# Kernel tuning notes

Measured on AMD Instinct MI355X. Metric: run time of the kernel, lower is better.

Reference implementation:

```python
import jax, jax.numpy as jnp
import numpy as np

PATCH_NUMS = (1, 2, 3, 4, 5, 6, 8, 10, 13, 16)
B = 8
NUM_HEADS = 24
HEAD_DIM = 64
C = NUM_HEADS * HEAD_DIM  # 1536
ROPE_BASE = 10000.0


def _position_ids(batch):
    # Mirrors get_position_ids: 2D grid coords per scale, rescaled to the largest grid.
    largest = PATCH_NUMS[-1]
    coords = []
    for pn in PATCH_NUMS:
        g = np.stack(np.meshgrid(np.arange(pn), np.arange(pn), indexing='ij'), axis=-1)
        coords.append((g.astype(np.float64) / pn * largest).reshape(-1, 2))
    pos = np.concatenate(coords, axis=0).astype(np.float32)  # [L, 2]
    return jnp.asarray(np.broadcast_to(pos, (batch,) + pos.shape))


def setup_inputs() -> dict:
    key = jax.random.key(0)
    k0, k1, k2 = jax.random.split(key, 3)
    L = sum(p * p for p in PATCH_NUMS)  # 680
    s = 0.02
    return {
        'x': jax.random.normal(k0, (B, L, C), jnp.float32),
        'pos_ids': _position_ids(B),                                   # [B, L, 2] float coords
        'w_qkv': jax.random.normal(k1, (3 * C, C), jnp.float32) * s,   # fused QKV weight (no bias in Linear)
        'q_bias': jnp.zeros((C,), jnp.float32),                        # learnable q bias
        'v_bias': jnp.zeros((C,), jnp.float32),                        # learnable v bias (k bias is fixed zero)
        'w_o': jax.random.normal(k2, (C, C), jnp.float32) * s,
        'b_o': jnp.zeros((C,), jnp.float32),
    }


def _rope_2d_cos_sin(pos_ids):
    # LlamaRotaryEmbedding (2D): inv_freq over head_dim with step 4; each spatial axis
    # gets head_dim/2 rotary channels laid out as [fx, fx, fy, fy] (rotate-half pairing).
    inv_freq = 1.0 / (ROPE_BASE ** (jnp.arange(0, HEAD_DIM, 4, dtype=jnp.float32) / HEAD_DIM))  # [hd/4]
    f = pos_ids[..., None] * inv_freq                      # [B, L, 2, hd/4]
    f2 = jnp.concatenate([f, f], axis=-1)                  # [B, L, 2, hd/2]
    emb = f2.reshape(f2.shape[0], f2.shape[1], HEAD_DIM)   # [B, L, hd]
    return jnp.cos(emb), jnp.sin(emb)


def _rotate_half(t):
    h = t.shape[-1] // 2
    return jnp.concatenate([-t[..., h:], t[..., :h]], axis=-1)


def reference(x, pos_ids, w_qkv, q_bias, v_bias, w_o, b_o):
    Bb, L, Cc = x.shape
    bias = jnp.concatenate([q_bias, jnp.zeros_like(q_bias), v_bias])  # zero k bias
    qkv = (x @ w_qkv.T + bias).reshape(Bb, L, 3, NUM_HEADS, HEAD_DIM)
    q, k, v = qkv[:, :, 0], qkv[:, :, 1], qkv[:, :, 2]  # bshd

    cos, sin = _rope_2d_cos_sin(pos_ids)                # [B, L, hd]
    cos = cos[:, :, None, :]                            # broadcast over heads (unsqueeze_dim=2)
    sin = sin[:, :, None, :]
    q = q * cos + _rotate_half(q) * sin
    k = k * cos + _rotate_half(k) * sin

    scale = 1.0 / jnp.sqrt(jnp.asarray(HEAD_DIM, jnp.float32))
    scores = jnp.einsum('bshd,bthd->bhst', q, k) * scale  # [B, H, L, L]
    attn = jax.nn.softmax(scores, axis=-1)
    out = jnp.einsum('bhst,bthd->bshd', attn, v).reshape(Bb, L, Cc)
    return out @ w_o.T + b_o
```

## Files before the change

### kernel.cpp

```cpp
#include <hip/hip_runtime.h>
#include <cmath>

typedef _Float16 f16;
typedef _Float16 f16x2 __attribute__((ext_vector_type(2)));
typedef _Float16 f16x4 __attribute__((ext_vector_type(4)));
typedef _Float16 f16x8 __attribute__((ext_vector_type(8)));
typedef float f32x4 __attribute__((ext_vector_type(4)));

namespace {

constexpr int kB = 8;
constexpr int kL = 680;
constexpr int kH = 24;
constexpr int kD = 64;
constexpr int kC = 1536;
constexpr int kM = kB * kL;
constexpr int kN3 = 3 * kC;
constexpr int kNKT = 11;
constexpr int kNQT = 6;

#define ASYNC_CP16(gp, lp)                                          \
  __builtin_amdgcn_global_load_lds(                                 \
      (const __attribute__((address_space(1))) unsigned int*)(gp),  \
      (__attribute__((address_space(3))) unsigned int*)(lp), 16, 0, 0)

__device__ inline int xcd_swizzle(int bid, int nwg) {
  int q = nwg >> 3, r = nwg & 7;
  int x = bid & 7, idx = bid >> 3;
  return (x < r ? x * (q + 1) : r * (q + 1) + (x - r) * q) + idx;
}

__device__ inline void stripe_decode(int id, int gx, int gy, int& mt,
                                     int& nt) {
  const int SW = 4;
  int nst = (gx + SW - 1) / SW;
  int s = id / (gy * SW);
  if (s > nst - 1) s = nst - 1;
  int rem = id - s * gy * SW;
  int w = gx - s * SW;
  if (w > SW) w = SW;
  mt = rem / w;
  nt = s * SW + rem % w;
}

__global__ void fused_cvt_bias(const float* __restrict__ x,
                               const float* __restrict__ wqkv,
                               const float* __restrict__ wo,
                               const float* __restrict__ qb,
                               const float* __restrict__ vb,
                               f16* __restrict__ x16,
                               f16* __restrict__ wqkv16,
                               f16* __restrict__ wo16,
                               float* __restrict__ bias) {
  const int c0 = kM * kC / 4, c1 = kN3 * kC / 4, c2 = kC * kC / 4,
            c3 = kN3 / 4;
  int i = blockIdx.x * blockDim.x + threadIdx.x;
  const float* src = nullptr;
  f16* dst = nullptr;
  if (i < c0) {
    src = x; dst = x16;
  } else if ((i -= c0) < c1) {
    src = wqkv; dst = wqkv16;
  } else if ((i -= c1) < c2) {
    src = wo; dst = wo16;
  } else if ((i -= c2) < c3) {
    int base = i * 4;
    float vv[4];
#pragma unroll
    for (int k2 = 0; k2 < 4; ++k2) {
      int idx = base + k2;
      float b = 0.0f;
      if (idx < kC) b = qb[idx];
      else if (idx >= 2 * kC) b = vb[idx - 2 * kC];
      vv[k2] = b;
    }
    *reinterpret_cast<float4*>(&bias[base]) =
        make_float4(vv[0], vv[1], vv[2], vv[3]);
    return;
  } else {
    return;
  }
  float4 v = *reinterpret_cast<const float4*>(&src[i * 4]);
  f16x4 o;
  o[0] = (f16)v.x; o[1] = (f16)v.y; o[2] = (f16)v.z; o[3] = (f16)v.w;
  *reinterpret_cast<f16x4*>(&dst[i * 4]) = o;
}

__global__ void reduce_add(float* __restrict__ out,
                           const float* __restrict__ part, int n4) {
  int i = blockIdx.x * blockDim.x + threadIdx.x;
  if (i >= n4) return;
  float4 a = *reinterpret_cast<const float4*>(&out[i * 4]);
  float4 b = *reinterpret_cast<const float4*>(&part[i * 4]);
  a.x += b.x; a.y += b.y; a.z += b.z; a.w += b.w;
  *reinterpret_cast<float4*>(&out[i * 4]) = a;
}

template <typename OutT, bool ROPE>
__global__ __launch_bounds__(512, 2) void gemm256_8ph(
    const f16* __restrict__ A, const f16* __restrict__ Bw,
    const float* __restrict__ bias0, OutT* __restrict__ Cm0,
    OutT* __restrict__ Cm1, const float* __restrict__ pos, int M, int N,
    int K, int tHalf) {
  constexpr int HALF = 8192;
  constexpr int ABUF = 2 * HALF;
  constexpr int BUF = 2 * ABUF;
  __shared__ __align__(16) f16 sm[2 * BUF];

  const int tid = threadIdx.x;
  const int w = tid >> 6;
  const int lane = tid & 63;
  const int lr = lane & 15;
  const int quad = lane >> 4;
  const int wr = w >> 2;
  const int wc = w & 3;
  const int gx = gridDim.x;
  const int sw = xcd_swizzle(blockIdx.y * gx + blockIdx.x, gx * gridDim.y);
  int mt, nt;
  stripe_decode(sw, gx, gridDim.y, mt, nt);
  const int m0 = mt * 256;
  const int n0 = nt * 256;

  const int NTall = K >> 6;
  int tS = 0, tE = NTall;
  OutT* Cm = Cm0;
  const float* bias = bias0;
  if (gridDim.z == 2) {
    if (blockIdx.z == 1) {
      tS = tHalf;
      Cm = Cm1;
      bias = nullptr;
    } else {
      tE = tHalf;
    }
  }
  const int NTt = tE - tS;

  const f16* aptr[2][2];
  const f16* bptr[2][2];
  int dstoff0 = tid * 8;
  int dstoff1 = (tid + 512) * 8;
#pragma unroll
  for (int h = 0; h < 2; ++h) {
#pragma unroll
    for (int n = 0; n < 2; ++n) {
      int idx = n * 512 + tid;
      int kb = idx >> 7, r = idx & 127;
      int ra = m0 + h * 128 + r;
      if (ra > M - 1) ra = M - 1;
      aptr[h][n] = A + (size_t)ra * K + kb * 8;
      bptr[h][n] = Bw + (size_t)(n0 + h * 128 + r) * K + kb * 8;
    }
  }

  auto stageA = [&](int t, int h, int q) {
    f16* d = &sm[q * BUF + h * HALF];
    ASYNC_CP16(aptr[h][0] + t * 64, &d[dstoff0]);
    ASYNC_CP16(aptr[h][1] + t * 64, &d[dstoff1]);
  };
  auto stageB = [&](int t, int h, int q) {
    f16* d = &sm[q * BUF + ABUF + h * HALF];
    ASYNC_CP16(bptr[h][0] + t * 64, &d[dstoff0]);
    ASYNC_CP16(bptr[h][1] + t * 64, &d[dstoff1]);
  };

  f32x4 acc[8][4];
#pragma unroll
  for (int i = 0; i < 8; ++i)
#pragma unroll
    for (int j = 0; j < 4; ++j)
#pragma unroll
      for (int c = 0; c < 4; ++c) acc[i][j][c] = 0.0f;

  const int bRow0 = (wc & 1) * 64;

  stageA(tS, 0, 0);
  stageA(tS, 1, 0);
  stageB(tS, 0, 0);
  stageB(tS, 1, 0);
  stageB(tS + 1, 0, 1);
  stageB(tS + 1, 1, 1);
  asm volatile("s_waitcnt vmcnt(4)" ::: "memory");
  __builtin_amdgcn_s_barrier();

  const int NIT = NTt >> 1;
  for (int itr = 0; itr < NIT; ++itr) {
    const int tt0 = itr * 2;
#pragma unroll
    for (int hf = 0; hf < 2; ++hf) {
      const int tcur = tS + tt0 + hf;
      const int ta = tcur + 1;
      const int tb = tcur + 2;
      const f16* Aq = &sm[hf * BUF + wr * HALF];
      const f16* Bq = &sm[hf * BUF + ABUF + (wc >> 1) * HALF];
      f16x8 a0[4], a1[4], b0[4], b1[4];

#pragma unroll
      for (int i = 0; i < 4; ++i)
        a0[i] = *reinterpret_cast<const f16x8*>(
            &Aq[((quad << 7) + i * 16 + lr) * 8]);
#pragma unroll
      for (int j = 0; j < 4; ++j)
        b0[j] = *reinterpret_cast<const f16x8*>(
            &Bq[((quad << 7) + bRow0 + j * 16 + lr) * 8]);
      if (ta < tE) stageA(ta, 0, hf ^ 1);
      __builtin_amdgcn_s_barrier();
      asm volatile("s_waitcnt lgkmcnt(0)" ::: "memory");
      __builtin_amdgcn_s_setprio(1);
#pragma unroll
      for (int i = 0; i < 4; ++i)
#pragma unroll
        for (int j = 0; j < 4; ++j)
          acc[i][j] = __builtin_amdgcn_mfma_f32_16x16x32_f16(
              a0[i], b0[j], acc[i][j], 0, 0, 0);
      __builtin_amdgcn_s_setprio(0);
      __builtin_amdgcn_s_barrier();

#pragma unroll
      for (int j = 0; j < 4; ++j)
        b1[j] = *reinterpret_cast<const f16x8*>(
            &Bq[(((4 + quad) << 7) + bRow0 + j * 16 + lr) * 8]);
#pragma unroll
      for (int i = 0; i < 4; ++i)
        a1[i] = *reinterpret_cast<const f16x8*>(
            &Aq[((quad << 7) + (i + 4) * 16 + lr) * 8]);
      if (ta < tE) stageA(ta, 1, hf ^ 1);
      __builtin_amdgcn_s_barrier();
      asm volatile("s_waitcnt lgkmcnt(0)" ::: "memory");
      __builtin_amdgcn_s_setprio(1);
#pragma unroll
      for (int i = 0; i < 4; ++i)
#pragma unroll
        for (int j = 0; j < 4; ++j)
          acc[i + 4][j] = __builtin_amdgcn_mfma_f32_16x16x32_f16(
              a1[i], b0[j], acc[i + 4][j], 0, 0, 0);
      __builtin_amdgcn_s_setprio(0);
      __builtin_amdgcn_s_barrier();

#pragma unroll
      for (int i = 0; i < 4; ++i)
        a0[i] = *reinterpret_cast<const f16x8*>(
            &Aq[(((4 + quad) << 7) + i * 16 + lr) * 8]);
      if (tb < tE) stageB(tb, 0, hf);
      __builtin_amdgcn_s_barrier();
      asm volatile("s_waitcnt lgkmcnt(0)" ::: "memory");
      __builtin_amdgcn_s_setprio(1);
#pragma unroll
      for (int i = 0; i < 4; ++i)
#pragma unroll
        for (int j = 0; j < 4; ++j)
          acc[i][j] = __builtin_amdgcn_mfma_f32_16x16x32_f16(
              a0[i], b1[j], acc[i][j], 0, 0, 0);
      __builtin_amdgcn_s_setprio(0);
      __builtin_amdgcn_s_barrier();

#pragma unroll
      for (int i = 0; i < 4; ++i)
        a1[i] = *reinterpret_cast<const f16x8*>(
            &Aq[(((4 + quad) << 7) + (i + 4) * 16 + lr) * 8]);
      if (tb < tE) stageB(tb, 1, hf);
      __builtin_amdgcn_s_barrier();
      asm volatile("s_waitcnt lgkmcnt(0)" ::: "memory");
      __builtin_amdgcn_s_setprio(1);
#pragma unroll
      for (int i = 0; i < 4; ++i)
#pragma unroll
        for (int j = 0; j < 4; ++j)
          acc[i + 4][j] = __builtin_amdgcn_mfma_f32_16x16x32_f16(
              a1[i], b1[j], acc[i + 4][j], 0, 0, 0);
      __builtin_amdgcn_s_setprio(0);
      if (tb < tE)
        asm volatile("s_waitcnt vmcnt(4)" ::: "memory");
      else
        asm volatile("s_waitcnt vmcnt(0)" ::: "memory");
      __builtin_amdgcn_s_barrier();
    }
  }

  float bv[4];
#pragma unroll
  for (int j = 0; j < 4; ++j)
    bv[j] = bias ? bias[n0 + wc * 64 + j * 16 + lr] : 0.0f;

  if (ROPE && n0 < 2 * kC) {
    const float fr = exp2f(-(float)lr * (13.287712379549449f / 16.0f));
#pragma unroll
    for (int i = 0; i < 8; ++i) {
#pragma unroll
      for (int r = 0; r < 4; ++r) {
        int row = m0 + wr * 128 + i * 16 + quad * 4 + r;
        if (row < M) {
          float a0r = pos[row * 2 + 0] * fr;
          float a1r = pos[row * 2 + 1] * fr;
          float s0 = __sinf(a0r), c0 = __cosf(a0r);
          float s1 = __sinf(a1r), c1 = __cosf(a1r);
#pragma unroll
          for (int j = 0; j < 2; ++j) {
            float v0 = acc[i][j][r] + bv[j];
            float v1 = acc[i][j + 2][r] + bv[j + 2];
            int col = n0 + wc * 64 + j * 16 + lr;
            Cm[(size_t)row * N + col] = (OutT)(v0 * c0 - v1 * s0);
            Cm[(size_t)row * N + col + 32] = (OutT)(v1 * c1 + v0 * s1);
          }
        }
      }
    }
  } else {
#pragma unroll
    for (int i = 0; i < 8; ++i) {
#pragma unroll
      for (int j = 0; j < 4; ++j) {
#pragma unroll
        for (int r = 0; r < 4; ++r) {
          int row = m0 + wr * 128 + i * 16 + quad * 4 + r;
          if (row < M) {
            int col = n0 + wc * 64 + j * 16 + lr;
            Cm[(size_t)row * N + col] = (OutT)(acc[i][j][r] + bv[j]);
          }
        }
      }
    }
  }
}

__global__ __launch_bounds__(256, 3) void attn_mfma(
    const f16* __restrict__ qkv, f16* __restrict__ attnout) {
  __shared__ __align__(16) f16 Ks[64 * 72];
  __shared__ __align__(16) f16 Vts[64 * 72];
  __shared__ __align__(16) f16 Pl[4][32 * 72];

  const int tid = threadIdx.x;
  const int w = tid >> 6;
  const int lane = tid & 63;
  const int lr = lane & 15;
  const int qd = lane >> 4;

  const int bid = blockIdx.x;
  const int xcd = bid & 7;
  const int rest = bid >> 3;
  const int qt = rest % kNQT;
  const int g = xcd + 8 * (rest / kNQT);
  const int h = g % kH;
  const int b = g / kH;
  const int q0 = qt * 128;

  f16x8 aq[2][2];
#pragma unroll
  for (int rt = 0; rt < 2; ++rt) {
    int qrow = q0 + w * 32 + rt * 16 + lr;
    if (qrow > kL - 1) qrow = kL - 1;
    const f16* qp = qkv + (size_t)(b * kL + qrow) * kN3 + h * kD;
#pragma unroll
    for (int ks = 0; ks < 2; ++ks)
      aq[rt][ks] =
          *reinterpret_cast<const f16x8*>(qp + ks * 32 + qd * 8);
  }

  const int kkey0 = tid >> 3, kdc = tid & 7;
  const int kkey1 = (tid + 256) >> 3;
  const int vkey0 = (tid & 31) * 2;
  const int vd0 = (tid >> 5) * 8;

  f16x8 kpre0, kpre1, vpre0, vpre1;
  auto prefetch = [&](int kt0) {
    int kg0 = kt0 + kkey0;
    if (kg0 > kL - 1) kg0 = kL - 1;
    kpre0 = *reinterpret_cast<const f16x8*>(
        qkv + (size_t)(b * kL + kg0) * kN3 + kC + h * kD + kdc * 8);
    int kg1 = kt0 + kkey1;
    if (kg1 > kL - 1) kg1 = kL - 1;
    kpre1 = *reinterpret_cast<const f16x8*>(
        qkv + (size_t)(b * kL + kg1) * kN3 + kC + h * kD + kdc * 8);
    int vg0 = kt0 + vkey0;
    if (vg0 > kL - 1) vg0 = kL - 1;
    vpre0 = *reinterpret_cast<const f16x8*>(
        qkv + (size_t)(b * kL + vg0) * kN3 + 2 * kC + h * kD + vd0);
    int vg1 = kt0 + vkey0 + 1;
    if (vg1 > kL - 1) vg1 = kL - 1;
    vpre1 = *reinterpret_cast<const f16x8*>(
        qkv + (size_t)(b * kL + vg1) * kN3 + 2 * kC + h * kD + vd0);
  };
  prefetch(0);

  f32x4 o_acc[2][4];
#pragma unroll
  for (int rt = 0; rt < 2; ++rt)
#pragma unroll
    for (int nt = 0; nt < 4; ++nt)
#pragma unroll
      for (int r = 0; r < 4; ++r) o_acc[rt][nt][r] = 0.0f;
  float lsum[2][4] = {{0.f, 0.f, 0.f, 0.f}, {0.f, 0.f, 0.f, 0.f}};

  for (int it = 0; it < kNKT; ++it) {
    const int kt0 = it * 64;
    __syncthreads();

    *reinterpret_cast<f16x8*>(&Ks[kkey0 * 72 + kdc * 8]) = kpre0;
    *reinterpret_cast<f16x8*>(&Ks[kkey1 * 72 + kdc * 8]) = kpre1;
#pragma unroll
    for (int i = 0; i < 8; ++i) {
      f16x2 pr;
      pr[0] = vpre0[i];
      pr[1] = vpre1[i];
      *reinterpret_cast<f16x2*>(&Vts[(vd0 + i) * 72 + vkey0]) = pr;
    }
    prefetch((it < kNKT - 1) ? (it + 1) * 64 : it * 64);
    __syncthreads();

    f32x4 s_acc[2][4];
#pragma unroll
    for (int rt = 0; rt < 2; ++rt)
#pragma unroll
      for (int t = 0; t < 4; ++t)
#pragma unroll
        for (int r = 0; r < 4; ++r) s_acc[rt][t][r] = 0.0f;
#pragma unroll
    for (int ks = 0; ks < 2; ++ks) {
#pragma unroll
      for (int t = 0; t < 4; ++t) {
        f16x8 bk = *reinterpret_cast<const f16x8*>(
            &Ks[(t * 16 + lr) * 72 + ks * 32 + qd * 8]);
        s_acc[0][t] = __builtin_amdgcn_mfma_f32_16x16x32_f16(
            aq[0][ks], bk, s_acc[0][t], 0, 0, 0);
        s_acc[1][t] = __builtin_amdgcn_mfma_f32_16x16x32_f16(
            aq[1][ks], bk, s_acc[1][t], 0, 0, 0);
      }
    }

#pragma unroll
    for (int rt = 0; rt < 2; ++rt) {
#pragma unroll
      for (int t = 0; t < 4; ++t) {
        const bool valid = (kt0 + t * 16 + lr) < kL;
#pragma unroll
        for (int r = 0; r < 4; ++r) {
          float p = valid ? __expf(s_acc[rt][t][r] * 0.125f) : 0.0f;
          lsum[rt][r] += p;
          Pl[w][(rt * 16 + qd * 4 + r) * 72 + t * 16 + lr] = (f16)p;
        }
      }
    }

#pragma unroll
    for (int ks = 0; ks < 2; ++ks) {
      f16x8 ap[2];
#pragma unroll
      for (int rt = 0; rt < 2; ++rt)
        ap[rt] = *reinterpret_cast<const f16x8*>(
            &Pl[w][(rt * 16 + lr) * 72 + ks * 32 + qd * 8]);
#pragma unroll
      for (int nt = 0; nt < 4; ++nt) {
        f16x8 bv = *reinterpret_cast<const f16x8*>(
            &Vts[(nt * 16 + lr) * 72 + ks * 32 + qd * 8]);
        o_acc[0][nt] = __builtin_amdgcn_mfma_f32_16x16x32_f16(
            ap[0], bv, o_acc[0][nt], 0, 0, 0);
        o_acc[1][nt] = __builtin_amdgcn_mfma_f32_16x16x32_f16(
            ap[1], bv, o_acc[1][nt], 0, 0, 0);
      }
    }
  }

#pragma unroll
  for (int rt = 0; rt < 2; ++rt)
#pragma unroll
    for (int r = 0; r < 4; ++r) {
#pragma unroll
      for (int m = 1; m < 16; m <<= 1)
        lsum[rt][r] += __shfl_xor(lsum[rt][r], m, 64);
    }

#pragma unroll
  for (int rt = 0; rt < 2; ++rt) {
#pragma unroll
    for (int nt = 0; nt < 4; ++nt) {
#pragma unroll
      for (int r = 0; r < 4; ++r) {
        int qr = q0 + w * 32 + rt * 16 + qd * 4 + r;
        if (qr < kL) {
          attnout[(size_t)(b * kL + qr) * kC + h * kD + nt * 16 + lr] =
              (f16)(o_acc[rt][nt][r] / lsum[rt][r]);
        }
      }
    }
  }
}

}

extern "C" void kernel_launch(void* const* d_in, const int* in_sizes, int n_in,
                              void* d_out, int out_size, void* d_ws,
                              size_t ws_size, hipStream_t stream) {
  const float* x = (const float*)d_in[0];
  const float* pos = (const float*)d_in[1];
  const float* w_qkv = (const float*)d_in[2];
  const float* q_bias = (const float*)d_in[3];
  const float* v_bias = (const float*)d_in[4];
  const float* w_o = (const float*)d_in[5];
  const float* b_o = (const float*)d_in[6];
  float* out = (float*)d_out;

  f16* qkv16 = (f16*)d_ws;
  f16* x16 = qkv16 + (size_t)kM * kN3;
  f16* wqkv16 = x16 + (size_t)kM * kC;
  f16* wo16 = wqkv16 + (size_t)kN3 * kC;
  f16* ao16 = wo16 + (size_t)kC * kC;
  float* bias_full = (float*)(ao16 + (size_t)kM * kC);
  float* proj_part = (float*)d_ws;

  {
    const int c0 = kM * kC / 4, c1 = kN3 * kC / 4, c2 = kC * kC / 4,
              c3 = kN3 / 4;
    int nchunks = c0 + c1 + c2 + c3;
    fused_cvt_bias<<<(nchunks + 255) / 256, 256, 0, stream>>>(
        x, w_qkv, w_o, q_bias, v_bias, x16, wqkv16, wo16, bias_full);
  }
  gemm256_8ph<f16, true><<<dim3(kN3 / 256, (kM + 255) / 256, 1), 512, 0,
                           stream>>>(x16, wqkv16, bias_full, qkv16, nullptr,
                                     pos, kM, kN3, kC, 0);
  attn_mfma<<<dim3(kNQT * kH * kB), 256, 0, stream>>>(qkv16, ao16);
  gemm256_8ph<float, false><<<dim3(kC / 256, (kM + 255) / 256, 2), 512, 0,
                              stream>>>(ao16, wo16, b_o, out, proj_part,
                                        nullptr, kM, kC, kC, 12);
  reduce_add<<<(kM * kC / 4 + 255) / 256, 256, 0, stream>>>(out, proj_part,
                                                            kM * kC / 4);
}
```

Baseline: 406.0 us.

## Drop split-K output projection and restructure GEMM inner loop into two phases

Removes the split-K launch of the output-projection GEMM, along with its partial-sum buffer and the separate reduce_add kernel, so each tile computes the full K range and writes the final output directly. The GEMM main loop now runs two phases per K-tile instead of four: each phase loads all eight A fragments and one B fragment, issues 32 MFMAs, and stages both halves of the next A or B tile at once. This cuts barriers and the extra reduction pass, in exchange for higher register pressure and half as many blocks in the output projection (6x22 grid), which lowers occupancy on a large GPU.

```diff
diff --git a/kernel.cpp b/kernel.cpp
--- a/kernel.cpp
+++ b/kernel.cpp
@@ -86,22 +86,11 @@
   *reinterpret_cast<f16x4*>(&dst[i * 4]) = o;
 }
 
-__global__ void reduce_add(float* __restrict__ out,
-                           const float* __restrict__ part, int n4) {
-  int i = blockIdx.x * blockDim.x + threadIdx.x;
-  if (i >= n4) return;
-  float4 a = *reinterpret_cast<const float4*>(&out[i * 4]);
-  float4 b = *reinterpret_cast<const float4*>(&part[i * 4]);
-  a.x += b.x; a.y += b.y; a.z += b.z; a.w += b.w;
-  *reinterpret_cast<float4*>(&out[i * 4]) = a;
-}
-
 template <typename OutT, bool ROPE>
 __global__ __launch_bounds__(512, 2) void gemm256_8ph(
     const f16* __restrict__ A, const f16* __restrict__ Bw,
-    const float* __restrict__ bias0, OutT* __restrict__ Cm0,
-    OutT* __restrict__ Cm1, const float* __restrict__ pos, int M, int N,
-    int K, int tHalf) {
+    const float* __restrict__ bias, OutT* __restrict__ Cm,
+    const float* __restrict__ pos, int M, int N, int K) {
   constexpr int HALF = 8192;
   constexpr int ABUF = 2 * HALF;
   constexpr int BUF = 2 * ABUF;
@@ -120,21 +109,7 @@
   stripe_decode(sw, gx, gridDim.y, mt, nt);
   const int m0 = mt * 256;
   const int n0 = nt * 256;
-
-  const int NTall = K >> 6;
-  int tS = 0, tE = NTall;
-  OutT* Cm = Cm0;
-  const float* bias = bias0;
-  if (gridDim.z == 2) {
-    if (blockIdx.z == 1) {
-      tS = tHalf;
-      Cm = Cm1;
-      bias = nullptr;
-    } else {
-      tE = tHalf;
-    }
-  }
-  const int NTt = tE - tS;
+  const int NT = K >> 6;
 
   const f16* aptr[2][2];
   const f16* bptr[2][2];
@@ -174,36 +149,43 @@
 
   const int bRow0 = (wc & 1) * 64;
 
-  stageA(tS, 0, 0);
-  stageA(tS, 1, 0);
-  stageB(tS, 0, 0);
-  stageB(tS, 1, 0);
-  stageB(tS + 1, 0, 1);
-  stageB(tS + 1, 1, 1);
+  stageA(0, 0, 0);
+  stageA(0, 1, 0);
+  stageB(0, 0, 0);
+  stageB(0, 1, 0);
+  stageB(1, 0, 1);
+  stageB(1, 1, 1);
   asm volatile("s_waitcnt vmcnt(4)" ::: "memory");
   __builtin_amdgcn_s_barrier();
 
-  const int NIT = NTt >> 1;
+  const int NIT = NT >> 1;
   for (int itr = 0; itr < NIT; ++itr) {
-    const int tt0 = itr * 2;
+    const int t0 = itr * 2;
 #pragma unroll
     for (int hf = 0; hf < 2; ++hf) {
-      const int tcur = tS + tt0 + hf;
+      const int tcur = t0 + hf;
       const int ta = tcur + 1;
       const int tb = tcur + 2;
       const f16* Aq = &sm[hf * BUF + wr * HALF];
       const f16* Bq = &sm[hf * BUF + ABUF + (wc >> 1) * HALF];
-      f16x8 a0[4], a1[4], b0[4], b1[4];
+      f16x8 a0[4], a1[4], bb[4];
 
 #pragma unroll
       for (int i = 0; i < 4; ++i)
         a0[i] = *reinterpret_cast<const f16x8*>(
             &Aq[((quad << 7) + i * 16 + lr) * 8]);
 #pragma unroll
+      for (int i = 0; i < 4; ++i)
+        a1[i] = *reinterpret_cast<const f16x8*>(
+            &Aq[((quad << 7) + (i + 4) * 16 + lr) * 8]);
+#pragma unroll
       for (int j = 0; j < 4; ++j)
-        b0[j] = *reinterpret_cast<const f16x8*>(
+        bb[j] = *reinterpret_cast<const f16x8*>(
             &Bq[((quad << 7) + bRow0 + j * 16 + lr) * 8]);
-      if (ta < tE) stageA(ta, 0, hf ^ 1);
+      if (ta < NT) {
+        stageA(ta, 0, hf ^ 1);
+        stageA(ta, 1, hf ^ 1);
+      }
       __builtin_amdgcn_s_barrier();
       asm volatile("s_waitcnt lgkmcnt(0)" ::: "memory");
       __builtin_amdgcn_s_setprio(1);
@@ -212,19 +194,32 @@
 #pragma unroll
         for (int j = 0; j < 4; ++j)
           acc[i][j] = __builtin_amdgcn_mfma_f32_16x16x32_f16(
-              a0[i], b0[j], acc[i][j], 0, 0, 0);
+              a0[i], bb[j], acc[i][j], 0, 0, 0);
+#pragma unroll
+      for (int i = 0; i < 4; ++i)
+#pragma unroll
+        for (int j = 0; j < 4; ++j)
+          acc[i + 4][j] = __builtin_amdgcn_mfma_f32_16x16x32_f16(
+              a1[i], bb[j], acc[i + 4][j], 0, 0, 0);
       __builtin_amdgcn_s_setprio(0);
       __builtin_amdgcn_s_barrier();
 
 #pragma unroll
+      for (int i = 0; i < 4; ++i)
+        a0[i] = *reinterpret_cast<const f16x8*>(
+            &Aq[(((4 + quad) << 7) + i * 16 + lr) * 8]);
+#pragma unroll
+      for (int i = 0; i < 4; ++i)
+        a1[i] = *reinterpret_cast<const f16x8*>(
+            &Aq[(((4 + quad) << 7) + (i + 4) * 16 + lr) * 8]);
+#pragma unroll
       for (int j = 0; j < 4; ++j)
-        b1[j] = *reinterpret_cast<const f16x8*>(
+        bb[j] = *reinterpret_cast<const f16x8*>(
             &Bq[(((4 + quad) << 7) + bRow0 + j * 16 + lr) * 8]);
-#pragma unroll
-      for (int i = 0; i < 4; ++i)
-        a1[i] = *reinterpret_cast<const f16x8*>(
-            &Aq[((quad << 7) + (i + 4) * 16 + lr) * 8]);
-      if (ta < tE) stageA(ta, 1, hf ^ 1);
+      if (tb < NT) {
+        stageB(tb, 0, hf);
+        stageB(tb, 1, hf);
+      }
       __builtin_amdgcn_s_barrier();
       asm volatile("s_waitcnt lgkmcnt(0)" ::: "memory");
       __builtin_amdgcn_s_setprio(1);
@@ -232,44 +227,16 @@
       for (int i = 0; i < 4; ++i)
 #pragma unroll
         for (int j = 0; j < 4; ++j)
-          acc[i + 4][j] = __builtin_amdgcn_mfma_f32_16x16x32_f16(
-              a1[i], b0[j], acc[i + 4][j], 0, 0, 0);
-      __builtin_amdgcn_s_setprio(0);
-      __builtin_amdgcn_s_barrier();
-
-#pragma unroll
-      for (int i = 0; i < 4; ++i)
-        a0[i] = *reinterpret_cast<const f16x8*>(
-            &Aq[(((4 + quad) << 7) + i * 16 + lr) * 8]);
-      if (tb < tE) stageB(tb, 0, hf);
-      __builtin_amdgcn_s_barrier();
-      asm volatile("s_waitcnt lgkmcnt(0)" ::: "memory");
-      __builtin_amdgcn_s_setprio(1);
-#pragma unroll
-      for (int i = 0; i < 4; ++i)
-#pragma unroll
-        for (int j = 0; j < 4; ++j)
           acc[i][j] = __builtin_amdgcn_mfma_f32_16x16x32_f16(
-              a0[i], b1[j], acc[i][j], 0, 0, 0);
-      __builtin_amdgcn_s_setprio(0);
-      __builtin_amdgcn_s_barrier();
-
-#pragma unroll
-      for (int i = 0; i < 4; ++i)
-        a1[i] = *reinterpret_cast<const f16x8*>(
-            &Aq[(((4 + quad) << 7) + (i + 4) * 16 + lr) * 8]);
-      if (tb < tE) stageB(tb, 1, hf);
-      __builtin_amdgcn_s_barrier();
-      asm volatile("s_waitcnt lgkmcnt(0)" ::: "memory");
-      __builtin_amdgcn_s_setprio(1);
+              a0[i], bb[j], acc[i][j], 0, 0, 0);
 #pragma unroll
       for (int i = 0; i < 4; ++i)
 #pragma unroll
         for (int j = 0; j < 4; ++j)
           acc[i + 4][j] = __builtin_amdgcn_mfma_f32_16x16x32_f16(
-              a1[i], b1[j], acc[i + 4][j], 0, 0, 0);
+              a1[i], bb[j], acc[i + 4][j], 0, 0, 0);
       __builtin_amdgcn_s_setprio(0);
-      if (tb < tE)
+      if (tb < NT)
         asm volatile("s_waitcnt vmcnt(4)" ::: "memory");
       else
         asm volatile("s_waitcnt vmcnt(0)" ::: "memory");
@@ -279,8 +246,7 @@
 
   float bv[4];
 #pragma unroll
-  for (int j = 0; j < 4; ++j)
-    bv[j] = bias ? bias[n0 + wc * 64 + j * 16 + lr] : 0.0f;
+  for (int j = 0; j < 4; ++j) bv[j] = bias[n0 + wc * 64 + j * 16 + lr];
 
   if (ROPE && n0 < 2 * kC) {
     const float fr = exp2f(-(float)lr * (13.287712379549449f / 16.0f));
@@ -505,7 +471,6 @@
   f16* wo16 = wqkv16 + (size_t)kN3 * kC;
   f16* ao16 = wo16 + (size_t)kC * kC;
   float* bias_full = (float*)(ao16 + (size_t)kM * kC);
-  float* proj_part = (float*)d_ws;
 
   {
     const int c0 = kM * kC / 4, c1 = kN3 * kC / 4, c2 = kC * kC / 4,
@@ -514,13 +479,11 @@
     fused_cvt_bias<<<(nchunks + 255) / 256, 256, 0, stream>>>(
         x, w_qkv, w_o, q_bias, v_bias, x16, wqkv16, wo16, bias_full);
   }
-  gemm256_8ph<f16, true><<<dim3(kN3 / 256, (kM + 255) / 256, 1), 512, 0,
-                           stream>>>(x16, wqkv16, bias_full, qkv16, nullptr,
-                                     pos, kM, kN3, kC, 0);
+  gemm256_8ph<f16, true><<<dim3(kN3 / 256, (kM + 255) / 256), 512, 0,
+                           stream>>>(x16, wqkv16, bias_full, qkv16, pos, kM,
+                                     kN3, kC);
   attn_mfma<<<dim3(kNQT * kH * kB), 256, 0, stream>>>(qkv16, ao16);
-  gemm256_8ph<float, false><<<dim3(kC / 256, (kM + 255) / 256, 2), 512, 0,
-                              stream>>>(ao16, wo16, b_o, out, proj_part,
-                                        nullptr, kM, kC, kC, 12);
-  reduce_add<<<(kM * kC / 4 + 255) / 256, 256, 0, stream>>>(out, proj_part,
-                                                            kM * kC / 4);
-}
+  gemm256_8ph<float, false><<<dim3(kC / 256, (kM + 255) / 256), 512, 0,
+                              stream>>>(ao16, wo16, b_o, out, nullptr, kM, kC,
+                                        kC);
+}
```

After: 455.2 us. 1.12x slower.
